# Kernel optimization log

Hardware: AMD Instinct MI355X
Metric: run time of the kernel (lower is better)

## Reference

```python
import jax, jax.numpy as jnp
import numpy as np

# ContextualAttention config (matches init_kwargs)
KS, STRIDE, DIL, FUSE_K, SCALE = 3, 1, 1, 3, 10.0
B, C, H, W = 2, 128, 64, 64
L = H * W  # number of background patches (SAME padding, stride 1)


def _same_pad(x, k, s):
    # TF-style SAME padding, identical to the repo's same_padding helper
    _, _, h, w = x.shape
    oh, ow = -(-h // s), -(-w // s)
    ph = max(0, (oh - 1) * s + k - h)
    pw = max(0, (ow - 1) * s + k - w)
    return jnp.pad(x, ((0, 0), (0, 0), (ph // 2, ph - ph // 2), (pw // 2, pw - pw // 2)))


def _patches(x, k, s):
    # extract_image_patches: SAME pad + unfold -> [N, L, C*k*k], (c, kh, kw) ordering
    xp = _same_pad(x, k, s)
    n, c, hp, wp = xp.shape
    oh, ow = (hp - k) // s + 1, (wp - k) // s + 1
    cols = jnp.stack(
        [xp[:, :, i:i + (oh - 1) * s + 1:s, j:j + (ow - 1) * s + 1:s]
         for i in range(k) for j in range(k)], axis=2)  # [N, C, k*k, oh, ow]
    return cols.reshape(n, c * k * k, oh * ow).transpose(0, 2, 1)


def _fuse(scores):
    # diagonal fuse-smoothing: conv the [L_b, L_f] score matrix with eye(k), twice
    # (second pass on the transposed spatial layout), exactly as in the torch code
    bn = scores.shape[0]
    eye = jnp.eye(FUSE_K, dtype=scores.dtype)[None, None]  # [1,1,k,k]
    conv = lambda v: jax.lax.conv_general_dilated(
        v, eye, (1, 1), [(1, 1), (1, 1)],
        dimension_numbers=('NCHW', 'OIHW', 'NCHW'))
    y = conv(scores.reshape(bn, 1, L, L))
    y = y.reshape(bn, H, W, H, W).transpose(0, 2, 1, 4, 3).reshape(bn, 1, L, L)
    y = conv(y)
    y = y.reshape(bn, W, H, W, H).transpose(0, 2, 1, 4, 3)  # back to [b,H,W,H,W]
    return y.reshape(bn, L, H, W)


def setup_inputs() -> dict:
    key = jax.random.key(0)
    kf, kb, km = jax.random.split(key, 3)
    f = jax.random.normal(kf, (B, C, H, W), jnp.float32)
    b = jax.random.normal(kb, (B, C, H, W), jnp.float32)
    mask = (jax.random.uniform(km, (1, 1, H, W)) < 0.05).astype(jnp.float32)
    return {"f": f, "b": b, "mask": mask}


def reference(f, b, mask):
    kernel = 2 * DIL  # raw patch size for aggregation (=2)
    # raw background patches used by the transposed-conv aggregation
    raw_w = _patches(b, kernel, DIL * STRIDE).reshape(B, L, C, kernel, kernel)
    # DIL == 1 => F.interpolate(scale=1.0, nearest) is identity on f/b/mask
    w = _patches(b, KS, STRIDE)      # [B, L, C*9] matching patches
    fp = _patches(f, KS, 1)          # [B, Lf, C*9] foreground patches (SAME pad)
    m = _patches(mask, KS, STRIDE)[0]                    # [L, 9]
    mm = (jnp.mean(m, axis=1) == 0.0).astype(f.dtype)    # [L] 1 = patch usable

    # per-patch L2 normalization (clamped at 1e-4), conv-as-similarity == patch GEMM
    wn = w / jnp.maximum(jnp.sqrt(jnp.sum(w * w, axis=2, keepdims=True)), 1e-4)
    scores = jnp.einsum('bkd,bqd->bkq', wn, fp).reshape(B, L, H, W)
    scores = _fuse(scores)

    mmb = mm[None, :, None, None]
    attn = jax.nn.softmax(scores * mmb * SCALE, axis=1) * mmb  # softmax over L

    # conv_transpose2d(attn, raw_w, stride=1, padding=1) == VALID corr with flipped,
    # IO-swapped 2x2 kernel (k-1-p = 0 padding); per-sample weights -> vmap
    def agg(a, rw):  # a: [L,H,W], rw: [L,C,2,2]
        rhs = jnp.flip(rw, axis=(2, 3)).transpose(1, 0, 2, 3)  # [C, L, 2, 2] OIHW
        return jax.lax.conv_general_dilated(
            a[None], rhs, (1, 1), [(0, 0), (0, 0)],
            dimension_numbers=('NCHW', 'OIHW', 'NCHW'))[0]

    y = jax.vmap(agg)(attn, raw_w) / 4.0       # [B, C, H-1, W-1]
    y = jnp.pad(y, ((0, 0), (0, 0), (0, 1), (0, 1)))  # output_padding = DIL % 2 = 1
    return y
```

## Files before the change

kernel.cpp:

```cpp
#include <hip/hip_runtime.h>

#define L 4096
#define HH 64
#define CC 128
#define BB 2

typedef _Float16 f16;
typedef _Float16 f16x8 __attribute__((ext_vector_type(8)));
typedef float f32x4 __attribute__((ext_vector_type(4)));

__device__ __forceinline__ void gl_lds16(const f16* g, f16* l) {
  __builtin_amdgcn_global_load_lds(
      (const __attribute__((address_space(1))) void*)g,
      (__attribute__((address_space(3))) void*)l, 16, 0, 0);
}

__device__ __forceinline__ int sigma_(int j) { return ((j & 63) << 6) | (j >> 6); }

__device__ float fuse9(const f16* __restrict__ Sb, int k, int j) {
  float acc = 0.f;
  int cK = sigma_(k), cQ = sigma_(j);
#pragma unroll
  for (int u = -1; u <= 1; ++u) {
    int a = cK + u, bq = cQ + u;
    if ((unsigned)a < L && (unsigned)bq < L) {
      int r = sigma_(a), c = sigma_(bq);
#pragma unroll
      for (int t = -1; t <= 1; ++t) {
        int rr = r + t, cc = c + t;
        if ((unsigned)rr < L && (unsigned)cc < L) acc += (float)Sb[(size_t)rr * L + cc];
      }
    }
  }
  return acc;
}

__global__ __launch_bounds__(256) void k_repack(
    const float* __restrict__ b, const float* __restrict__ f,
    f16* __restrict__ bT, f16* __restrict__ fT, f16* __restrict__ zp) {
  __shared__ float tile[128][65];
  int u0 = blockIdx.x * 64;
  int z = blockIdx.y;
  int batch = z >> 1;
  const float* src = ((z & 1) ? f : b) + (size_t)batch * CC * L;
  f16* dst = ((z & 1) ? fT : bT) + (size_t)batch * L * CC;
  int tid = threadIdx.x;
  if (blockIdx.x == 0 && z == 0 && tid < 32) zp[tid] = (f16)0.f;
#pragma unroll
  for (int i = 0; i < 32; ++i) {
    int idx = i * 256 + tid;
    int c = idx >> 6, ux = idx & 63;
    tile[c][ux] = src[(size_t)c * L + u0 + ux];
  }
  __syncthreads();
#pragma unroll
  for (int j = 0; j < 4; ++j) {
    int t2 = j * 256 + tid;
    int u = t2 >> 4, ch = t2 & 15;
    f16x8 v;
#pragma unroll
    for (int e = 0; e < 8; ++e) v[e] = (f16)tile[ch * 8 + e][u];
    *(f16x8*)(dst + (size_t)(u0 + u) * CC + ch * 8) = v;
  }
}

__global__ __launch_bounds__(256) void k_ssq(const float* __restrict__ b, float* __restrict__ ssq) {
  int u = blockIdx.x * 256 + threadIdx.x;
  int batch = blockIdx.y;
  const float* bp = b + (size_t)batch * CC * L + u;
  float s = 0.f;
#pragma unroll 4
  for (int c = 0; c < CC; ++c) { float v = bp[(size_t)c * L]; s += v * v; }
  ssq[batch * L + u] = s;
}

__global__ void k_norm(const float* __restrict__ ssq, float* __restrict__ inv_n) {
  int gi = blockIdx.x * 256 + threadIdx.x;
  if (gi >= BB * L) return;
  int batch = gi >> 12, k = gi & (L - 1);
  int ky = k >> 6, kx = k & 63;
  float s = 0.f;
#pragma unroll
  for (int dy = -1; dy <= 1; ++dy)
#pragma unroll
    for (int dx = -1; dx <= 1; ++dx) {
      if ((unsigned)(ky + dy) < 64 && (unsigned)(kx + dx) < 64)
        s += ssq[batch * L + k + dy * 64 + dx];
    }
  inv_n[gi] = 1.f / fmaxf(sqrtf(s), 1e-4f);
}

__global__ __launch_bounds__(256) void k_prep_bm(const float* __restrict__ b, f16* __restrict__ bm) {
  int idx = blockIdx.x * 256 + threadIdx.x;
  int e8 = idx * 8;
  int k0 = e8 & (L - 1);
  int c = (e8 >> 12) & (CC - 1);
  int bt = e8 >> 19;
  int batch = bt & 1;
  int tap = bt >> 1;
  int di = 1 - (tap >> 1), dj = 1 - (tap & 1);
  int ky = k0 >> 6, kx0 = k0 & 63;
  const float* src = b + ((size_t)batch * CC + c) * L + k0 + di * 64 + dj;
  bool rowok = (ky + di) < 64;
  f16x8 v;
#pragma unroll
  for (int e = 0; e < 8; ++e) {
    float x = (rowok && (kx0 + e + dj) < 64) ? src[e] : 0.f;
    v[e] = (f16)x;
  }
  *(f16x8*)(bm + (size_t)e8) = v;
}

__global__ void k_prep_mm(const float* __restrict__ mask, float* __restrict__ mmv) {
  int k = blockIdx.x * 256 + threadIdx.x;
  if (k >= L) return;
  int ky = k >> 6, kx = k & 63;
  float s = 0.f;
  for (int i = 0; i < 3; ++i)
    for (int j = 0; j < 3; ++j) {
      int yy = ky + i - 1, xx = kx + j - 1;
      if (yy >= 0 && yy < 64 && xx >= 0 && xx < 64) s += mask[yy * 64 + xx];
    }
  mmv[k] = (s == 0.f) ? 1.f : 0.f;
}

__global__ __launch_bounds__(256) void k_gemm_scores(
    const f16* __restrict__ bT, const f16* __restrict__ fT,
    const float* __restrict__ inv_n, const f16* __restrict__ zp,
    f16* __restrict__ S) {
  __shared__ f16 As[2][128 * 64];
  __shared__ f16 Bs[2][128 * 64];
  int qt = blockIdx.x, kt = blockIdx.y, batch = blockIdx.z;
  int tid = threadIdx.x, wid = tid >> 6, lane = tid & 63;
  int wr = wid >> 1, wc = wid & 1;
  const f16* A0 = bT + (size_t)batch * L * CC;
  const f16* B0 = fT + (size_t)batch * L * CC;
  f32x4 acc[4][4] = {};
  int rA = wr * 64 + (lane & 15);
  int rB = wc * 64 + (lane & 15);

  const f16* baseA_[4]; const f16* baseB_[4];
  int offL_[4];
  unsigned mA_[4], mB_[4];
#pragma unroll
  for (int i = 0; i < 4; ++i) {
    int chunk = (i * 4 + wid) * 64 + lane;
    int row = chunk >> 3;
    int lg = (lane & 7) ^ (row & 7);
    int k = kt * 128 + row;
    int q = qt * 128 + row;
    baseA_[i] = A0 + (size_t)k * CC + lg * 8;
    baseB_[i] = B0 + (size_t)q * CC + lg * 8;
    offL_[i] = chunk * 8;
    int ky = k >> 6, kx = k & 63, qy = q >> 6, qx = q & 63;
    unsigned ma = 0, mb = 0;
#pragma unroll
    for (int rr = 0; rr < 9; ++rr) {
      int dy = rr / 3 - 1, dx = rr - (rr / 3) * 3 - 1;
      if ((unsigned)(ky + dy) < 64u && (unsigned)(kx + dx) < 64u) ma |= 1u << rr;
      if ((unsigned)(qy + dy) < 64u && (unsigned)(qx + dx) < 64u) mb |= 1u << rr;
    }
    mA_[i] = ma; mB_[i] = mb;
  }

#define STAGE_T(tt, bsel)                                                     \
  do {                                                                        \
    int rr_ = (tt) >> 1, half_ = (tt) & 1;                                    \
    int dy_ = rr_ / 3 - 1, dx_ = rr_ - (rr_ / 3) * 3 - 1;                     \
    int doff_ = (dy_ * 64 + dx_) * CC + half_ * 64;                           \
    _Pragma("unroll")                                                         \
    for (int i = 0; i < 4; ++i) {                                             \
      gl_lds16(((mA_[i] >> rr_) & 1u) ? (baseA_[i] + doff_) : zp,             \
               &As[bsel][0] + offL_[i]);                                      \
      gl_lds16(((mB_[i] >> rr_) & 1u) ? (baseB_[i] + doff_) : zp,             \
               &Bs[bsel][0] + offL_[i]);                                      \
    }                                                                         \
  } while (0)

  STAGE_T(0, 0);
  int cur = 0;
#pragma unroll 1
  for (int t = 0; t < 18; ++t) {
    __syncthreads();
    if (t < 17) STAGE_T(t + 1, cur ^ 1);
    const f16* Ab = &As[cur][0];
    const f16* Bb = &Bs[cur][0];
#pragma unroll
    for (int h2 = 0; h2 < 2; ++h2) {
      int cb = h2 * 4 + (lane >> 4);
      f16x8 af[4], bf[4];
#pragma unroll
      for (int m = 0; m < 4; ++m) {
        int row = rA + m * 16;
        af[m] = *(const f16x8*)(Ab + row * 64 + ((cb ^ (row & 7)) * 8));
      }
#pragma unroll
      for (int n = 0; n < 4; ++n) {
        int row = rB + n * 16;
        bf[n] = *(const f16x8*)(Bb + row * 64 + ((cb ^ (row & 7)) * 8));
      }
#pragma unroll
      for (int m = 0; m < 4; ++m)
#pragma unroll
        for (int n = 0; n < 4; ++n)
          acc[m][n] = __builtin_amdgcn_mfma_f32_16x16x32_f16(af[m], bf[n], acc[m][n], 0, 0, 0);
    }
    cur ^= 1;
  }
#undef STAGE_T

  f16* Srow = S + (size_t)batch * L * L;
  int kbase = kt * 128 + wr * 64 + (lane >> 4) * 4;
  int qbase = qt * 128 + wc * 64 + (lane & 15);
#pragma unroll
  for (int m = 0; m < 4; ++m) {
    f32x4 invv = *(const f32x4*)(inv_n + (size_t)batch * L + kbase + m * 16);
#pragma unroll
    for (int r = 0; r < 4; ++r) {
      f16* dst = Srow + (size_t)(kbase + m * 16 + r) * L + qbase;
#pragma unroll
      for (int n = 0; n < 4; ++n) dst[n * 16] = (f16)(acc[m][n][r] * invv[r]);
    }
  }
}

__global__ __launch_bounds__(256) void k_fuse_stats(
    const f16* __restrict__ S, const float* __restrict__ mmv,
    float* __restrict__ T3, float* __restrict__ pm, float* __restrict__ pl) {
  int tid = threadIdx.x;
  if (tid >= 247) return;
  int jc = blockIdx.x, kc = blockIdx.y, batch = blockIdx.z;
  int g = jc * 247 + tid;
  int q0 = 72 + g * 8;
  const f16* Sb = S + (size_t)batch * L * L;
  float* Tb = T3 + (size_t)batch * L * L;
  float m8[8], l8[8];
#pragma unroll
  for (int e = 0; e < 8; ++e) { m8[e] = -3.0e38f; l8[e] = 0.f; }
  int cnt = 0;
  int k0 = kc * 16;
  for (int kk = 0; kk < 16; ++kk) {
    int k = k0 + kk;
    if (mmv[k] == 0.f) { ++cnt; continue; }
    float acc[8] = {0.f, 0.f, 0.f, 0.f, 0.f, 0.f, 0.f, 0.f};
    int cK = sigma_(k);
#pragma unroll
    for (int u = -1; u <= 1; ++u) {
      int a = cK + u;
      if ((unsigned)a >= L) continue;
      int r = sigma_(a);
      const f16* cb = Sb + (size_t)r * L + (q0 + 64 * u);
      {
        f16x8 v = *(const f16x8*)cb;
#pragma unroll
        for (int e = 0; e < 8; ++e) acc[e] += (float)v[e];
      }
      if (r >= 1) {
        const f16* rm = cb - L;
        f16x8 v = *(const f16x8*)rm;
        acc[0] += (float)rm[-1];
#pragma unroll
        for (int e = 1; e < 8; ++e) acc[e] += (float)v[e - 1];
      }
      if (r <= L - 2) {
        const f16* rp = cb + L;
        f16x8 v = *(const f16x8*)rp;
#pragma unroll
        for (int e = 0; e < 7; ++e) acc[e] += (float)v[e + 1];
        acc[7] += (float)rp[8];
      }
    }
#pragma unroll
    for (int e = 0; e < 8; ++e) acc[e] *= 10.f;
    float* trow = Tb + (size_t)k * L + q0;
    *(f32x4*)trow = *(f32x4*)&acc[0];
    *(f32x4*)(trow + 4) = *(f32x4*)&acc[4];
#pragma unroll
    for (int e = 0; e < 8; ++e) {
      float nm = fmaxf(m8[e], acc[e]);
      l8[e] = l8[e] * __expf(m8[e] - nm) + __expf(acc[e] - nm);
      m8[e] = nm;
    }
  }
  float fc = (float)cnt;
  float om[8], ol[8];
#pragma unroll
  for (int e = 0; e < 8; ++e) {
    float nm = fmaxf(m8[e], 0.f);
    ol[e] = l8[e] * __expf(m8[e] - nm) + fc * __expf(-nm);
    om[e] = nm;
  }
  float* pmp = pm + (size_t)kc * (BB * L) + (size_t)batch * L + q0;
  float* plp = pl + (size_t)kc * (BB * L) + (size_t)batch * L + q0;
  *(f32x4*)pmp = *(f32x4*)&om[0]; *(f32x4*)(pmp + 4) = *(f32x4*)&om[4];
  *(f32x4*)plp = *(f32x4*)&ol[0]; *(f32x4*)(plp + 4) = *(f32x4*)&ol[4];
}

__global__ __launch_bounds__(256) void k_fuse_stats_edge(
    const f16* __restrict__ S, const float* __restrict__ mmv,
    float* __restrict__ T3, float* __restrict__ pm, float* __restrict__ pl) {
  int tid = threadIdx.x;
  if (tid >= 144) return;
  int q = (tid < 72) ? tid : (4024 + tid - 72);
  int kc = blockIdx.x, batch = blockIdx.y;
  const f16* Sb = S + (size_t)batch * L * L;
  float* Tb = T3 + (size_t)batch * L * L;
  float m = -3.0e38f, l = 0.f;
  int cnt = 0;
  int k0 = kc * 16;
  for (int kk = 0; kk < 16; ++kk) {
    int k = k0 + kk;
    if (mmv[k] == 0.f) { ++cnt; continue; }
    float logit = 10.f * fuse9(Sb, k, q);
    Tb[(size_t)k * L + q] = logit;
    float nm = fmaxf(m, logit);
    l = l * __expf(m - nm) + __expf(logit - nm);
    m = nm;
  }
  float nm = fmaxf(m, 0.f);
  l = l * __expf(m - nm) + (float)cnt * __expf(-nm);
  pm[(size_t)kc * (BB * L) + (size_t)batch * L + q] = nm;
  pl[(size_t)kc * (BB * L) + (size_t)batch * L + q] = l;
}

__global__ __launch_bounds__(256) void k_softmax_reduce(
    const float* __restrict__ pm, const float* __restrict__ pl,
    float* __restrict__ Mq, float* __restrict__ invLq) {
  __shared__ float sm[4][64], sl[4][64];
  int tid = threadIdx.x;
  int ql = tid & 63, part = tid >> 6;
  int qi = blockIdx.x * 64 + ql;
  float m = -3.0e38f, l = 0.f;
  int i0 = part * 64;
#pragma unroll 4
  for (int i = i0; i < i0 + 64; ++i) {
    float pmv = pm[(size_t)i * (BB * L) + qi];
    float plv = pl[(size_t)i * (BB * L) + qi];
    float nm = fmaxf(m, pmv);
    l = l * __expf(m - nm) + plv * __expf(pmv - nm);
    m = nm;
  }
  sm[part][ql] = m; sl[part][ql] = l;
  __syncthreads();
  if (part == 0) {
    float M = sm[0][ql];
#pragma unroll
    for (int p = 1; p < 4; ++p) M = fmaxf(M, sm[p][ql]);
    float Ls = 0.f;
#pragma unroll
    for (int p = 0; p < 4; ++p) Ls += sl[p][ql] * __expf(sm[p][ql] - M);
    Mq[qi] = M;
    invLq[qi] = 1.f / Ls;
  }
}

__global__ __launch_bounds__(512) void k_agg(
    const float* __restrict__ T3, const float* __restrict__ mmv,
    const float* __restrict__ Mq, const float* __restrict__ invLq,
    const f16* __restrict__ bm, float* __restrict__ part) {
  __shared__ f16 Asm[512 * 32];
  __shared__ f16 Bt[136 * 40];
  int pt = blockIdx.x, ks = blockIdx.y, batch = blockIdx.z;
  int p0 = pt * 64;
  int tid = threadIdx.x, wid = tid >> 6, lane = tid & 63;
  int wr = wid >> 1, wc = wid & 1;
  const float* Tb = T3 + (size_t)batch * L * L;
  const float* mq0 = Mq + (size_t)batch * L;
  const float* il0 = invLq + (size_t)batch * L;
  f32x4 acc[2][2] = {};
  int kend = ks * 1024 + 1024;
  for (int k0 = ks * 1024; k0 < kend; k0 += 32) {
    __syncthreads();
#pragma unroll
    for (int i = 0; i < 4; ++i) {
      int R = wid * 64 + i * 16 + (lane >> 2);
      int tap = R >> 7, c = R & 127;
      int chl = (lane & 3) ^ ((R >> 1) & 3);
      const f16* g = bm + (((size_t)(tap * 2 + batch) * CC + c) * L) + k0 + chl * 8;
      gl_lds16(g, Asm + R * 32 + (lane & 3) * 8);
    }
    for (int tau = tid; tau < 544; tau += 512) {
      int kk = tau / 17, ch = tau - kk * 17;
      int k = k0 + kk;
      int pbase = p0 + ch * 8;
      f16 v[8];
      if (mmv[k] != 0.f) {
        const float* trow = Tb + (size_t)k * L + pbase;
        if (pbase + 7 < L) {
          f32x4 t0 = *(const f32x4*)trow;
          f32x4 t1 = *(const f32x4*)(trow + 4);
          f32x4 m0 = *(const f32x4*)(mq0 + pbase);
          f32x4 m1 = *(const f32x4*)(mq0 + pbase + 4);
          f32x4 i0 = *(const f32x4*)(il0 + pbase);
          f32x4 i1 = *(const f32x4*)(il0 + pbase + 4);
#pragma unroll
          for (int e = 0; e < 4; ++e) v[e] = (f16)(__expf(t0[e] - m0[e]) * i0[e]);
#pragma unroll
          for (int e = 0; e < 4; ++e) v[4 + e] = (f16)(__expf(t1[e] - m1[e]) * i1[e]);
        } else {
#pragma unroll
          for (int e = 0; e < 8; ++e) {
            int q = pbase + e;
            v[e] = (q < L) ? (f16)(__expf(trow[e] - mq0[q]) * il0[q]) : (f16)0.f;
          }
        }
      } else {
#pragma unroll
        for (int e = 0; e < 8; ++e) v[e] = (f16)0.f;
      }
#pragma unroll
      for (int e = 0; e < 8; ++e) {
        int pp = ch * 8 + e;
        Bt[pp * 40 + (((kk >> 3) ^ ((pp >> 3) & 3)) * 8) + (kk & 7)] = v[e];
      }
    }
    __syncthreads();
#pragma unroll
    for (int tap = 0; tap < 4; ++tap) {
      int dlt = (tap >> 1) * 64 + (tap & 1);
      f16x8 af[2], bf[2];
#pragma unroll
      for (int m = 0; m < 2; ++m) {
        int R = tap * 128 + wr * 32 + m * 16 + (lane & 15);
        int ph = (lane >> 4) ^ ((R >> 1) & 3);
        af[m] = *(const f16x8*)(Asm + R * 32 + ph * 8);
      }
#pragma unroll
      for (int n = 0; n < 2; ++n) {
        int pp = wc * 32 + n * 16 + (lane & 15) + dlt;
        int ph = (lane >> 4) ^ ((pp >> 3) & 3);
        bf[n] = *(const f16x8*)(Bt + pp * 40 + ph * 8);
      }
#pragma unroll
      for (int m = 0; m < 2; ++m)
#pragma unroll
        for (int n = 0; n < 2; ++n)
          acc[m][n] = __builtin_amdgcn_mfma_f32_16x16x32_f16(af[m], bf[n], acc[m][n], 0, 0, 0);
    }
  }
  int cb = wr * 32 + (lane >> 4) * 4;
  int pb = p0 + wc * 32 + (lane & 15);
#pragma unroll
  for (int m = 0; m < 2; ++m)
#pragma unroll
    for (int n = 0; n < 2; ++n)
#pragma unroll
      for (int r = 0; r < 4; ++r) {
        int c = cb + m * 16 + r;
        int p = pb + n * 16;
        part[(((size_t)ks * 2 + batch) * CC + c) * L + p] = acc[m][n][r];
      }
}

__global__ __launch_bounds__(256) void k_agg_reduce(const float* __restrict__ part, float* __restrict__ out) {
  int idx = (blockIdx.x * 256 + threadIdx.x) * 4;
  f32x4 s = {0.f, 0.f, 0.f, 0.f};
#pragma unroll
  for (int ks = 0; ks < 4; ++ks) {
    f32x4 v = *(const f32x4*)(part + (size_t)ks * (2 * CC * L) + idx);
#pragma unroll
    for (int e = 0; e < 4; ++e) s[e] += v[e];
  }
  int p = idx & (L - 1);
  int u = p >> 6, vv = p & 63;
  f32x4 o;
#pragma unroll
  for (int e = 0; e < 4; ++e) o[e] = (u < 63 && (vv + e) < 63) ? s[e] * 0.25f : 0.f;
  *(f32x4*)(out + idx) = o;
}

extern "C" void kernel_launch(void* const* d_in, const int* in_sizes, int n_in,
                              void* d_out, int out_size, void* d_ws, size_t ws_size,
                              hipStream_t stream) {
  const float* f = (const float*)d_in[0];
  const float* b = (const float*)d_in[1];
  const float* mask = (const float*)d_in[2];
  float* out = (float*)d_out;
  char* ws = (char*)d_ws;

  float* T3  = (float*)(ws + 0);
  f16* S     = (f16*)(ws + 134217728);
  f16* bm    = (f16*)(ws + 201326592);
  float* part= (float*)(ws + 209715200);
  float* pm  = (float*)(ws + 226492416);
  float* pl  = (float*)(ws + 234881024);
  float* mmv = (float*)(ws + 243269632);
  float* Mq  = (float*)(ws + 243286016);
  float* iLq = (float*)(ws + 243318784);
  f16* bT    = (f16*)(ws + 243351552);
  f16* fT    = (f16*)(ws + 245448704);
  float* ssq = (float*)(ws + 247545856);
  float* invn= (float*)(ws + 247578624);
  f16* zp    = (f16*)(ws + 247611392);

  k_repack<<<dim3(64, 4), dim3(256), 0, stream>>>(b, f, bT, fT, zp);
  k_ssq<<<dim3(16, 2), dim3(256), 0, stream>>>(b, ssq);
  k_norm<<<dim3(32), dim3(256), 0, stream>>>(ssq, invn);
  k_prep_bm<<<dim3(2048), dim3(256), 0, stream>>>(b, bm);
  k_prep_mm<<<dim3(16), dim3(256), 0, stream>>>(mask, mmv);
  k_gemm_scores<<<dim3(32, 32, 2), dim3(256), 0, stream>>>(bT, fT, invn, zp, S);
  k_fuse_stats<<<dim3(2, 256, 2), dim3(256), 0, stream>>>(S, mmv, T3, pm, pl);
  k_fuse_stats_edge<<<dim3(256, 2), dim3(256), 0, stream>>>(S, mmv, T3, pm, pl);
  k_softmax_reduce<<<dim3(128), dim3(256), 0, stream>>>(pm, pl, Mq, iLq);
  k_agg<<<dim3(64, 4, 2), dim3(512), 0, stream>>>(T3, mmv, Mq, iLq, bm, part);
  k_agg_reduce<<<dim3(1024), dim3(256), 0, stream>>>(part, out);
}
```

Before: 321.0 us.

## Prefetch next attention tile into registers and vectorize LDS stores in k_agg

```diff
diff --git a/kernel.cpp b/kernel.cpp
--- a/kernel.cpp
+++ b/kernel.cpp
@@ -365,55 +365,70 @@
   int tid = threadIdx.x, wid = tid >> 6, lane = tid & 63;
   int wr = wid >> 1, wc = wid & 1;
   const float* Tb = T3 + (size_t)batch * L * L;
-  const float* mq0 = Mq + (size_t)batch * L;
-  const float* il0 = invLq + (size_t)batch * L;
+
+  const f16* gA_[4]; f16* lA_[4];
+#pragma unroll
+  for (int i = 0; i < 4; ++i) {
+    int R = wid * 64 + i * 16 + (lane >> 2);
+    int tap = R >> 7, c = R & 127;
+    int chl = (lane & 3) ^ ((R >> 1) & 3);
+    gA_[i] = bm + (((size_t)(tap * 2 + batch) * CC + c) * L) + chl * 8;
+    lA_[i] = Asm + R * 32 + (lane & 3) * 8;
+  }
+
+  bool act1 = (tid < 32);
+  int pp_[2], kg_[2]; bool qok_[2]; float M_[2], iL_[2];
+  const float* tb_[2]; f16* bw_[2];
+#pragma unroll
+  for (int s = 0; s < 2; ++s) {
+    int tau = tid + s * 512;
+    int ppv = tau % 136, kgv = tau / 136;
+    if (tau >= 544) { ppv = 0; kgv = 0; }
+    pp_[s] = ppv; kg_[s] = kgv;
+    int q = p0 + ppv;
+    bool qok = q < L;
+    int qc = qok ? q : (L - 1);
+    qok_[s] = qok;
+    M_[s] = Mq[(size_t)batch * L + qc];
+    iL_[s] = invLq[(size_t)batch * L + qc];
+    tb_[s] = Tb + (size_t)(kgv * 8) * L + qc;
+    bw_[s] = Bt + ppv * 40 + ((kgv ^ ((ppv >> 3) & 3)) * 8);
+  }
+
+  f16x8 vv_[2];
+  int kend = ks * 1024 + 1024;
+
+#define LOADB(K0)                                                             \
+  do {                                                                        \
+    _Pragma("unroll")                                                         \
+    for (int s = 0; s < 2; ++s) {                                             \
+      if (s == 1 && !act1) break;                                             \
+      const float* tp = tb_[s] + (size_t)(K0) * L;                            \
+      f32x4 ma = *(const f32x4*)(mmv + (K0) + kg_[s] * 8);                    \
+      f32x4 mb = *(const f32x4*)(mmv + (K0) + kg_[s] * 8 + 4);                \
+      float t[8];                                                             \
+      _Pragma("unroll")                                                       \
+      for (int j = 0; j < 8; ++j) t[j] = tp[(size_t)j * L];                   \
+      f16 v[8];                                                               \
+      _Pragma("unroll")                                                       \
+      for (int j = 0; j < 8; ++j) {                                           \
+        float mmj = (j < 4) ? ma[j] : mb[j - 4];                              \
+        v[j] = (qok_[s] && mmj != 0.f)                                        \
+                   ? (f16)(__expf(t[j] - M_[s]) * iL_[s]) : (f16)0.f;         \
+      }                                                                       \
+      vv_[s] = *(f16x8*)v;                                                    \
+    }                                                                         \
+  } while (0)
+
+  LOADB(ks * 1024);
   f32x4 acc[2][2] = {};
-  int kend = ks * 1024 + 1024;
+#pragma unroll 1
   for (int k0 = ks * 1024; k0 < kend; k0 += 32) {
     __syncthreads();
-#pragma unroll
-    for (int i = 0; i < 4; ++i) {
-      int R = wid * 64 + i * 16 + (lane >> 2);
-      int tap = R >> 7, c = R & 127;
-      int chl = (lane & 3) ^ ((R >> 1) & 3);
-      const f16* g = bm + (((size_t)(tap * 2 + batch) * CC + c) * L) + k0 + chl * 8;
-      gl_lds16(g, Asm + R * 32 + (lane & 3) * 8);
-    }
-    for (int tau = tid; tau < 544; tau += 512) {
-      int kk = tau / 17, ch = tau - kk * 17;
-      int k = k0 + kk;
-      int pbase = p0 + ch * 8;
-      f16 v[8];
-      if (mmv[k] != 0.f) {
-        const float* trow = Tb + (size_t)k * L + pbase;
-        if (pbase + 7 < L) {
-          f32x4 t0 = *(const f32x4*)trow;
-          f32x4 t1 = *(const f32x4*)(trow + 4);
-          f32x4 m0 = *(const f32x4*)(mq0 + pbase);
-          f32x4 m1 = *(const f32x4*)(mq0 + pbase + 4);
-          f32x4 i0 = *(const f32x4*)(il0 + pbase);
-          f32x4 i1 = *(const f32x4*)(il0 + pbase + 4);
-#pragma unroll
-          for (int e = 0; e < 4; ++e) v[e] = (f16)(__expf(t0[e] - m0[e]) * i0[e]);
-#pragma unroll
-          for (int e = 0; e < 4; ++e) v[4 + e] = (f16)(__expf(t1[e] - m1[e]) * i1[e]);
-        } else {
-#pragma unroll
-          for (int e = 0; e < 8; ++e) {
-            int q = pbase + e;
-            v[e] = (q < L) ? (f16)(__expf(trow[e] - mq0[q]) * il0[q]) : (f16)0.f;
-          }
-        }
-      } else {
-#pragma unroll
-        for (int e = 0; e < 8; ++e) v[e] = (f16)0.f;
-      }
-#pragma unroll
-      for (int e = 0; e < 8; ++e) {
-        int pp = ch * 8 + e;
-        Bt[pp * 40 + (((kk >> 3) ^ ((pp >> 3) & 3)) * 8) + (kk & 7)] = v[e];
-      }
-    }
+    *(f16x8*)bw_[0] = vv_[0];
+    if (act1) *(f16x8*)bw_[1] = vv_[1];
+#pragma unroll
+    for (int i = 0; i < 4; ++i) gl_lds16(gA_[i] + k0, lA_[i]);
     __syncthreads();
 #pragma unroll
     for (int tap = 0; tap < 4; ++tap) {
@@ -437,7 +452,10 @@
         for (int n = 0; n < 2; ++n)
           acc[m][n] = __builtin_amdgcn_mfma_f32_16x16x32_f16(af[m], bf[n], acc[m][n], 0, 0, 0);
     }
-  }
+    if (k0 + 32 < kend) LOADB(k0 + 32);
+  }
+#undef LOADB
+
   int cb = wr * 32 + (lane >> 4) * 4;
   int pb = p0 + wc * 32 + (lane & 15);
 #pragma unroll
```

After: 321.1 us. No clear change (+0.0%).
